# Performance work log

Hardware: AMD Instinct MI355X
Metric: run time of the kernel (lower is better)

The kernel has to match this reference:

```python
import jax, jax.numpy as jnp
import numpy as np

MAX_M = 16


def _twiddle(n, m):
    # exp(-2i*pi*n_a*m_a / (n*m)), shape (n, m), precomputed on host (static n, m)
    a = np.outer(np.arange(n), np.arange(m))
    return jnp.asarray(np.exp(-2j * np.pi * a / (n * m)).astype(np.complex64))


def _ref_dft_real(n, H):
    # reference DFT matrix as (H, n, n, 2) real view, matching ref_dft_matrix
    a = np.outer(np.arange(n), np.arange(n))
    M = np.exp(-2j * np.pi * a / n).astype(np.complex64)  # (n, n)
    M = np.broadcast_to(M, (H, n, n))
    return jnp.asarray(np.stack([M.real, M.imag], axis=-1).astype(np.float32))


def _cooley_tukey(k, n, m, mats):
    # k: (..., H, n*m) complex; mats[p]: (H, p, p) complex
    k = k.reshape(*k.shape[:-1], m, n)                      # (..., H, m, n)
    kf = jnp.einsum('hmo,...hon->...hmn', mats[m], k)       # m-length DFTs
    kf = jnp.einsum('nm,...mn->...nm', _twiddle(n, m), kf)  # twiddle + transpose -> (..., H, n, m)
    if n <= MAX_M:
        kf = jnp.einsum('hno,...hom->...hnm', mats[n], kf)  # n-length DFTs
    else:
        kf = jnp.moveaxis(kf, -1, -3)                        # '... h n m -> ... m h n'
        kf = _cooley_tukey(kf, n // MAX_M, MAX_M, mats)
        kf = jnp.moveaxis(kf, -3, -1)                        # '... m h n -> ... h n m'
    return kf.reshape(*kf.shape[:-2], n * m)


def block_fft(x, N, mats):
    # x: (..., H, L) complex, zero-pad to N, then recursive block FFT
    L = x.shape[-1]
    if L != N:
        x = jnp.pad(x, [(0, 0)] * (x.ndim - 1) + [(0, N - L)])
    return _cooley_tukey(x, N // MAX_M, MAX_M, mats)


def block_ifft(x, N, mats):
    return jnp.conj(block_fft(jnp.conj(x), N, mats)) / N


def setup_inputs() -> dict:
    key = jax.random.key(0)
    B, H, L = 16, 512, 1024
    ku, kk, kd = jax.random.split(key, 3)
    u = jax.random.normal(ku, (B, H, L), dtype=jnp.float32)
    k = jax.random.normal(kk, (H, L), dtype=jnp.float32) / L
    D = jax.random.normal(kd, (H,), dtype=jnp.float32)
    return {
        'u': u, 'k': k, 'D': D,
        'mat_2': _ref_dft_real(2, H),
        'mat_4': _ref_dft_real(4, H),
        'mat_8': _ref_dft_real(8, H),
        'mat_16': _ref_dft_real(16, H),
    }


def reference(u, k, D, mat_2, mat_4, mat_8, mat_16):
    cplx = lambda m: (m[..., 0] + 1j * m[..., 1]).astype(jnp.complex64)
    mats = {2: cplx(mat_2), 4: cplx(mat_4), 8: cplx(mat_8), 16: cplx(mat_16)}
    L = u.shape[-1]
    N = 2 * L  # causal FFT conv length
    k_f = block_fft(k.astype(jnp.complex64), N, mats)   # (H, N)
    u_f = block_fft(u.astype(jnp.complex64), N, mats)   # (B, H, N)
    y = block_ifft(u_f * k_f, N, mats)[..., :L].real    # (B, H, L)
    return (y + u * D[:, None]).astype(jnp.float32)
```

## Files before the change

### kernel.cpp

```cpp
#include <hip/hip_runtime.h>
#include <math.h>

#define NT     256
#define NB     16
#define NH     512
#define SEQ_L  1024
#define FFT_N  2048
#define RS     0.70710678118654752f

#define P(x) ((x) + ((x) >> 4))
#define BUF_SZ 2176

__device__ float2 g_kf[(size_t)NH * FFT_N];

__device__ __forceinline__ float2 cmul(float2 a, float2 b) {
    return make_float2(a.x * b.x - a.y * b.y, a.x * b.y + a.y * b.x);
}
__device__ __forceinline__ float2 cmulj(float2 a, float2 b) {
    return make_float2(a.x * b.x + a.y * b.y, a.y * b.x - a.x * b.y);
}
__device__ __forceinline__ float2 cadd(float2 a, float2 b) { return make_float2(a.x + b.x, a.y + b.y); }
__device__ __forceinline__ float2 csub(float2 a, float2 b) { return make_float2(a.x - b.x, a.y - b.y); }

template <int SIGN>
__device__ __forceinline__ void dft4(float2 x[4]) {
    float2 s0 = cadd(x[0], x[2]), s1 = csub(x[0], x[2]);
    float2 s2 = cadd(x[1], x[3]), s3 = csub(x[1], x[3]);
    x[0] = cadd(s0, s2);
    x[2] = csub(s0, s2);
    if (SIGN < 0) {
        x[1] = make_float2(s1.x + s3.y, s1.y - s3.x);
        x[3] = make_float2(s1.x - s3.y, s1.y + s3.x);
    } else {
        x[1] = make_float2(s1.x - s3.y, s1.y + s3.x);
        x[3] = make_float2(s1.x + s3.y, s1.y - s3.x);
    }
}

template <int SIGN>
__device__ __forceinline__ void dft8(float2 x[8]) {
    float2 e0 = cadd(x[0], x[4]), e1 = cadd(x[1], x[5]);
    float2 e2 = cadd(x[2], x[6]), e3 = cadd(x[3], x[7]);
    float2 o0 = csub(x[0], x[4]), o1 = csub(x[1], x[5]);
    float2 o2 = csub(x[2], x[6]), o3 = csub(x[3], x[7]);
    float2 t1, t2, t3;
    if (SIGN < 0) {
        t1 = make_float2(RS * (o1.x + o1.y), RS * (o1.y - o1.x));
        t2 = make_float2(o2.y, -o2.x);
        t3 = make_float2(-RS * (o3.x - o3.y), -RS * (o3.x + o3.y));
    } else {
        t1 = make_float2(RS * (o1.x - o1.y), RS * (o1.x + o1.y));
        t2 = make_float2(-o2.y, o2.x);
        t3 = make_float2(RS * (-o3.x - o3.y), RS * (o3.x - o3.y));
    }
    float2 s0 = cadd(e0, e2), s1 = csub(e0, e2), s2 = cadd(e1, e3), s3 = csub(e1, e3);
    x[0] = cadd(s0, s2);
    x[4] = csub(s0, s2);
    float2 u0 = cadd(o0, t2), u1 = csub(o0, t2), u2 = cadd(t1, t3), u3 = csub(t1, t3);
    x[1] = cadd(u0, u2);
    x[5] = csub(u0, u2);
    if (SIGN < 0) {
        x[2] = make_float2(s1.x + s3.y, s1.y - s3.x);
        x[6] = make_float2(s1.x - s3.y, s1.y + s3.x);
        x[3] = make_float2(u1.x + u3.y, u1.y - u3.x);
        x[7] = make_float2(u1.x - u3.y, u1.y + u3.x);
    } else {
        x[2] = make_float2(s1.x - s3.y, s1.y + s3.x);
        x[6] = make_float2(s1.x + s3.y, s1.y - s3.x);
        x[3] = make_float2(u1.x - u3.y, u1.y + u3.x);
        x[7] = make_float2(u1.x + u3.y, u1.y - u3.x);
    }
}

template <int SIGN>
__device__ __forceinline__ void stage8(float* re, float* im, const float2* tw,
                                       int t, int m, int twstep) {
    const int q = t & (m - 1);
    const int base = (t - q) * 8 + q;
    int idx[8];
    float2 x[8];
#pragma unroll
    for (int j = 0; j < 8; ++j) {
        idx[j] = P(base + j * m);
        x[j] = make_float2(re[idx[j]], im[idx[j]]);
    }
    const float2 w1 = tw[q * twstep];
    if (SIGN < 0) {
        dft8<-1>(x);
        float2 w = w1;
#pragma unroll
        for (int j = 1; j < 8; ++j) { x[j] = cmul(x[j], w); w = cmul(w, w1); }
    } else {
        float2 w = w1;
#pragma unroll
        for (int j = 1; j < 8; ++j) { x[j] = cmulj(x[j], w); w = cmul(w, w1); }
        dft8<+1>(x);
    }
#pragma unroll
    for (int j = 0; j < 8; ++j) { re[idx[j]] = x[j].x; im[idx[j]] = x[j].y; }
}

__device__ __forceinline__ void stage1_fwd(float* re, float* im, const float2* tw,
                                           int t, const float2 z[4]) {
    float2 e[4] = {z[0], z[1], z[2], z[3]};
    float2 o[4];
    o[0] = z[0];
    o[1] = make_float2(RS * (z[1].x + z[1].y), RS * (z[1].y - z[1].x));
    o[2] = make_float2(z[2].y, -z[2].x);
    o[3] = make_float2(-RS * (z[3].x - z[3].y), -RS * (z[3].x + z[3].y));
    dft4<-1>(e);
    dft4<-1>(o);
    float2 x[8] = {e[0], o[0], e[1], o[1], e[2], o[2], e[3], o[3]};
    const float2 w1 = tw[t];
    float2 w = w1;
#pragma unroll
    for (int j = 1; j < 8; ++j) { x[j] = cmul(x[j], w); w = cmul(w, w1); }
#pragma unroll
    for (int j = 0; j < 8; ++j) {
        const int id = P(t + j * 256);
        re[id] = x[j].x;
        im[id] = x[j].y;
    }
}

__global__ __launch_bounds__(NT, 8) void kfft_kernel(const float* __restrict__ kin) {
    __shared__ float re[BUF_SZ];
    __shared__ float im[BUF_SZ];
    __shared__ float2 tw[NT];
    const int t = threadIdx.x;
    const int h = blockIdx.x;
    {
        float sv, cv;
        sincosf(-6.283185307179586f * (float)t / (float)FFT_N, &sv, &cv);
        tw[t] = make_float2(cv, sv);
    }
    const float* krow = kin + (size_t)h * SEQ_L;
    float2 z[4];
#pragma unroll
    for (int l = 0; l < 4; ++l) z[l] = make_float2(krow[t + l * 256], 0.f);
    stage1_fwd(re, im, tw, t, z);
    __syncthreads();
    stage8<-1>(re, im, tw, t, 32, 8);
    __syncthreads();
    stage8<-1>(re, im, tw, t, 4, 64);
    __syncthreads();
    float2* out = g_kf + (size_t)h * FFT_N;
#pragma unroll
    for (int it = 0; it < 2; ++it) {
        const int b = t + it * NT;
        float2 x[4];
#pragma unroll
        for (int j = 0; j < 4; ++j) {
            const int id = P(4 * b + j);
            x[j] = make_float2(re[id], im[id]);
        }
        dft4<-1>(x);
#pragma unroll
        for (int j = 0; j < 4; ++j) out[4 * b + j] = x[j];
    }
}

__global__ __launch_bounds__(NT, 8) void conv_pair_kernel(const float* __restrict__ u,
                                                          const float* __restrict__ D,
                                                          float* __restrict__ out) {
    __shared__ float re[BUF_SZ];
    __shared__ float im[BUF_SZ];
    __shared__ float2 tw[NT];
    const int t = threadIdx.x;
    const int h = blockIdx.x & (NH - 1);
    const int bp = blockIdx.x >> 9;
    const size_t row0 = (size_t)(2 * bp) * NH + h;
    const size_t row1 = row0 + NH;
    {
        float sv, cv;
        sincosf(-6.283185307179586f * (float)t / (float)FFT_N, &sv, &cv);
        tw[t] = make_float2(cv, sv);
    }
    const float* u0 = u + row0 * SEQ_L;
    const float* u1 = u + row1 * SEQ_L;
    float ur0[4], ur1[4];
#pragma unroll
    for (int l = 0; l < 4; ++l) {
        ur0[l] = u0[t + l * 256];
        ur1[l] = u1[t + l * 256];
    }
    float2 z[4];
#pragma unroll
    for (int l = 0; l < 4; ++l) z[l] = make_float2(ur0[l], ur1[l]);
    stage1_fwd(re, im, tw, t, z);
    __syncthreads();
    stage8<-1>(re, im, tw, t, 32, 8);
    __syncthreads();
    stage8<-1>(re, im, tw, t, 4, 64);
    __syncthreads();
    const float2* kfr = g_kf + (size_t)h * FFT_N;
#pragma unroll
    for (int it = 0; it < 2; ++it) {
        const int b = t + it * NT;
        int id[4];
        float2 x[4];
#pragma unroll
        for (int j = 0; j < 4; ++j) {
            id[j] = P(4 * b + j);
            x[j] = make_float2(re[id[j]], im[id[j]]);
        }
        dft4<-1>(x);
#pragma unroll
        for (int j = 0; j < 4; ++j) x[j] = cmul(x[j], kfr[4 * b + j]);
        dft4<+1>(x);
#pragma unroll
        for (int j = 0; j < 4; ++j) { re[id[j]] = x[j].x; im[id[j]] = x[j].y; }
    }
    __syncthreads();
    stage8<+1>(re, im, tw, t, 4, 64);
    __syncthreads();
    stage8<+1>(re, im, tw, t, 32, 8);
    __syncthreads();
    float2 x[8];
#pragma unroll
    for (int j = 0; j < 8; ++j) {
        const int id = P(t + j * 256);
        x[j] = make_float2(re[id], im[id]);
    }
    {
        const float2 w1 = tw[t];
        float2 w = w1;
#pragma unroll
        for (int j = 1; j < 8; ++j) { x[j] = cmulj(x[j], w); w = cmul(w, w1); }
    }
    float2 e0 = cadd(x[0], x[4]), e1 = cadd(x[1], x[5]);
    float2 e2 = cadd(x[2], x[6]), e3 = cadd(x[3], x[7]);
    float2 o0 = csub(x[0], x[4]), o1 = csub(x[1], x[5]);
    float2 o2 = csub(x[2], x[6]), o3 = csub(x[3], x[7]);
    float2 t1 = make_float2(RS * (o1.x - o1.y), RS * (o1.x + o1.y));
    float2 t2 = make_float2(-o2.y, o2.x);
    float2 t3 = make_float2(RS * (-o3.x - o3.y), RS * (o3.x - o3.y));
    float2 s0 = cadd(e0, e2), s1 = csub(e0, e2), s2 = cadd(e1, e3), s3 = csub(e1, e3);
    float2 v0 = cadd(o0, t2), v1 = csub(o0, t2), v2 = cadd(t1, t3), v3 = csub(t1, t3);
    float2 y0 = cadd(s0, s2);
    float2 y1 = cadd(v0, v2);
    float2 y2 = make_float2(s1.x - s3.y, s1.y + s3.x);
    float2 y3 = make_float2(v1.x - v3.y, v1.y + v3.x);
    const float Dh = D[h];
    const float invN = 1.0f / (float)FFT_N;
    float* o0row = out + row0 * SEQ_L;
    float* o1row = out + row1 * SEQ_L;
    o0row[t]       = y0.x * invN + ur0[0] * Dh;
    o1row[t]       = y0.y * invN + ur1[0] * Dh;
    o0row[t + 256] = y1.x * invN + ur0[1] * Dh;
    o1row[t + 256] = y1.y * invN + ur1[1] * Dh;
    o0row[t + 512] = y2.x * invN + ur0[2] * Dh;
    o1row[t + 512] = y2.y * invN + ur1[2] * Dh;
    o0row[t + 768] = y3.x * invN + ur0[3] * Dh;
    o1row[t + 768] = y3.y * invN + ur1[3] * Dh;
}

extern "C" void kernel_launch(void* const* d_in, const int* in_sizes, int n_in,
                              void* d_out, int out_size, void* d_ws, size_t ws_size,
                              hipStream_t stream) {
    const float* u = (const float*)d_in[0];
    const float* k = (const float*)d_in[1];
    const float* D = (const float*)d_in[2];
    float* out = (float*)d_out;

    kfft_kernel<<<NH, NT, 0, stream>>>(k);
    conv_pair_kernel<<<NB * NH / 2, NT, 0, stream>>>(u, D, out);
}
```

Measured before the change: 118.6 us.

## Restructure FFT as radix-16x16x8 with 128 threads per block

Replaces the radix-8/8/8/4 staged FFT decomposition with a 16x16x8 factorization. The forward first stage exploits the zero padding, and the final inverse stage computes only the lower half of the outputs. Each thread now handles 16 points and block size drops from 256 to 128 threads, cutting the number of shared-memory passes and barriers. Kernel-spectrum reads and writes use float4. Costs include higher register pressure per thread and lower launch-bound occupancy.

```diff
diff --git a/kernel.cpp b/kernel.cpp
--- a/kernel.cpp
+++ b/kernel.cpp
@@ -1,17 +1,19 @@
 #include <hip/hip_runtime.h>
 #include <math.h>
 
-#define NT     256
+#define NT     128
 #define NB     16
 #define NH     512
 #define SEQ_L  1024
 #define FFT_N  2048
 #define RS     0.70710678118654752f
+#define C16    0.92387953251128675f
+#define S16    0.38268343236508977f
 
 #define P(x) ((x) + ((x) >> 4))
 #define BUF_SZ 2176
 
-__device__ float2 g_kf[(size_t)NH * FFT_N];
+__device__ __align__(16) float2 g_kf[(size_t)NH * FFT_N];
 
 __device__ __forceinline__ float2 cmul(float2 a, float2 b) {
     return make_float2(a.x * b.x - a.y * b.y, a.x * b.y + a.y * b.x);
@@ -73,186 +75,277 @@
 }
 
 template <int SIGN>
-__device__ __forceinline__ void stage8(float* re, float* im, const float2* tw,
-                                       int t, int m, int twstep) {
-    const int q = t & (m - 1);
-    const int base = (t - q) * 8 + q;
-    int idx[8];
-    float2 x[8];
-#pragma unroll
-    for (int j = 0; j < 8; ++j) {
-        idx[j] = P(base + j * m);
-        x[j] = make_float2(re[idx[j]], im[idx[j]]);
-    }
-    const float2 w1 = tw[q * twstep];
-    if (SIGN < 0) {
-        dft8<-1>(x);
-        float2 w = w1;
-#pragma unroll
-        for (int j = 1; j < 8; ++j) { x[j] = cmul(x[j], w); w = cmul(w, w1); }
-    } else {
-        float2 w = w1;
-#pragma unroll
-        for (int j = 1; j < 8; ++j) { x[j] = cmulj(x[j], w); w = cmul(w, w1); }
-        dft8<+1>(x);
-    }
-#pragma unroll
-    for (int j = 0; j < 8; ++j) { re[idx[j]] = x[j].x; im[idx[j]] = x[j].y; }
-}
-
-__device__ __forceinline__ void stage1_fwd(float* re, float* im, const float2* tw,
-                                           int t, const float2 z[4]) {
-    float2 e[4] = {z[0], z[1], z[2], z[3]};
-    float2 o[4];
-    o[0] = z[0];
-    o[1] = make_float2(RS * (z[1].x + z[1].y), RS * (z[1].y - z[1].x));
-    o[2] = make_float2(z[2].y, -z[2].x);
-    o[3] = make_float2(-RS * (z[3].x - z[3].y), -RS * (z[3].x + z[3].y));
-    dft4<-1>(e);
-    dft4<-1>(o);
-    float2 x[8] = {e[0], o[0], e[1], o[1], e[2], o[2], e[3], o[3]};
-    const float2 w1 = tw[t];
-    float2 w = w1;
-#pragma unroll
-    for (int j = 1; j < 8; ++j) { x[j] = cmul(x[j], w); w = cmul(w, w1); }
-#pragma unroll
-    for (int j = 0; j < 8; ++j) {
-        const int id = P(t + j * 256);
-        re[id] = x[j].x;
-        im[id] = x[j].y;
-    }
-}
-
-__global__ __launch_bounds__(NT, 8) void kfft_kernel(const float* __restrict__ kin) {
+__device__ __forceinline__ void dft16_twiddle(float2 v[4][4]) {
+    const float sg = (SIGN < 0) ? -1.f : 1.f;
+    const float2 W1 = make_float2(C16, sg * S16);
+    const float2 W2 = make_float2(RS, sg * RS);
+    const float2 W3 = make_float2(S16, sg * C16);
+    const float2 W6 = make_float2(-RS, sg * RS);
+    const float2 W9 = make_float2(-C16, -sg * S16);
+    v[1][1] = cmul(v[1][1], W1);
+    v[1][2] = cmul(v[1][2], W2);
+    v[1][3] = cmul(v[1][3], W3);
+    v[2][1] = cmul(v[2][1], W2);
+    v[2][2] = make_float2(-sg * v[2][2].y, sg * v[2][2].x);
+    v[2][3] = cmul(v[2][3], W6);
+    v[3][1] = cmul(v[3][1], W3);
+    v[3][2] = cmul(v[3][2], W6);
+    v[3][3] = cmul(v[3][3], W9);
+}
+
+template <int SIGN>
+__device__ __forceinline__ void dft16(float2 x[16]) {
+    float2 v[4][4];
+#pragma unroll
+    for (int n0 = 0; n0 < 4; ++n0) {
+        float2 a[4] = {x[n0], x[n0 + 4], x[n0 + 8], x[n0 + 12]};
+        dft4<SIGN>(a);
+        v[n0][0] = a[0]; v[n0][1] = a[1]; v[n0][2] = a[2]; v[n0][3] = a[3];
+    }
+    dft16_twiddle<SIGN>(v);
+#pragma unroll
+    for (int k0 = 0; k0 < 4; ++k0) {
+        float2 a[4] = {v[0][k0], v[1][k0], v[2][k0], v[3][k0]};
+        dft4<SIGN>(a);
+        x[k0] = a[0]; x[k0 + 4] = a[1]; x[k0 + 8] = a[2]; x[k0 + 12] = a[3];
+    }
+}
+
+__device__ __forceinline__ void dft16_zero8(const float2 z[8], float2 x[16]) {
+    float2 v[4][4];
+#pragma unroll
+    for (int n0 = 0; n0 < 4; ++n0) {
+        float2 a = z[n0], b = z[n0 + 4];
+        v[n0][0] = cadd(a, b);
+        v[n0][1] = make_float2(a.x + b.y, a.y - b.x);
+        v[n0][2] = csub(a, b);
+        v[n0][3] = make_float2(a.x - b.y, a.y + b.x);
+    }
+    dft16_twiddle<-1>(v);
+#pragma unroll
+    for (int k0 = 0; k0 < 4; ++k0) {
+        float2 a[4] = {v[0][k0], v[1][k0], v[2][k0], v[3][k0]};
+        dft4<-1>(a);
+        x[k0] = a[0]; x[k0 + 4] = a[1]; x[k0 + 8] = a[2]; x[k0 + 12] = a[3];
+    }
+}
+
+__device__ __forceinline__ void dft16_inv_low8(const float2 x[16], float2 y[8]) {
+    float2 v[4][4];
+#pragma unroll
+    for (int n0 = 0; n0 < 4; ++n0) {
+        float2 a[4] = {x[n0], x[n0 + 4], x[n0 + 8], x[n0 + 12]};
+        dft4<+1>(a);
+        v[n0][0] = a[0]; v[n0][1] = a[1]; v[n0][2] = a[2]; v[n0][3] = a[3];
+    }
+    dft16_twiddle<+1>(v);
+#pragma unroll
+    for (int k0 = 0; k0 < 4; ++k0) {
+        float2 x0 = v[0][k0], x1 = v[1][k0], x2 = v[2][k0], x3 = v[3][k0];
+        float2 s0 = cadd(x0, x2), s1 = csub(x0, x2);
+        float2 s2 = cadd(x1, x3), s3 = csub(x1, x3);
+        y[k0]     = cadd(s0, s2);
+        y[k0 + 4] = make_float2(s1.x - s3.y, s1.y + s3.x);
+    }
+}
+
+__global__ __launch_bounds__(NT, 4) void kfft_kernel(const float* __restrict__ kin) {
     __shared__ float re[BUF_SZ];
     __shared__ float im[BUF_SZ];
-    __shared__ float2 tw[NT];
+    __shared__ float2 twlds[NT];
     const int t = threadIdx.x;
     const int h = blockIdx.x;
+    float2 w1;
     {
         float sv, cv;
         sincosf(-6.283185307179586f * (float)t / (float)FFT_N, &sv, &cv);
-        tw[t] = make_float2(cv, sv);
+        w1 = make_float2(cv, sv);
+        twlds[t] = w1;
     }
     const float* krow = kin + (size_t)h * SEQ_L;
-    float2 z[4];
-#pragma unroll
-    for (int l = 0; l < 4; ++l) z[l] = make_float2(krow[t + l * 256], 0.f);
-    stage1_fwd(re, im, tw, t, z);
-    __syncthreads();
-    stage8<-1>(re, im, tw, t, 32, 8);
-    __syncthreads();
-    stage8<-1>(re, im, tw, t, 4, 64);
-    __syncthreads();
-    float2* out = g_kf + (size_t)h * FFT_N;
-#pragma unroll
-    for (int it = 0; it < 2; ++it) {
-        const int b = t + it * NT;
-        float2 x[4];
-#pragma unroll
-        for (int j = 0; j < 4; ++j) {
-            const int id = P(4 * b + j);
+    {
+        float2 z[8], x[16];
+#pragma unroll
+        for (int j = 0; j < 8; ++j) z[j] = make_float2(krow[t + 128 * j], 0.f);
+        dft16_zero8(z, x);
+        float2 w = w1;
+#pragma unroll
+        for (int c = 1; c < 16; ++c) { x[c] = cmul(x[c], w); w = cmul(w, w1); }
+#pragma unroll
+        for (int c = 0; c < 16; ++c) {
+            const int id = P(t + 128 * c);
+            re[id] = x[c].x; im[id] = x[c].y;
+        }
+    }
+    __syncthreads();
+    const int cblk = t >> 3, r = t & 7;
+    const int base = 128 * cblk + r;
+    {
+        float2 x[16];
+#pragma unroll
+        for (int j = 0; j < 16; ++j) {
+            const int id = P(base + 8 * j);
             x[j] = make_float2(re[id], im[id]);
         }
-        dft4<-1>(x);
-#pragma unroll
-        for (int j = 0; j < 4; ++j) out[4 * b + j] = x[j];
-    }
-}
-
-__global__ __launch_bounds__(NT, 8) void conv_pair_kernel(const float* __restrict__ u,
+        dft16<-1>(x);
+        const float2 ws = twlds[16 * r];
+        float2 w = ws;
+#pragma unroll
+        for (int c2 = 1; c2 < 16; ++c2) { x[c2] = cmul(x[c2], w); w = cmul(w, ws); }
+#pragma unroll
+        for (int c2 = 0; c2 < 16; ++c2) {
+            const int id = P(base + 8 * c2);
+            re[id] = x[c2].x; im[id] = x[c2].y;
+        }
+    }
+    __syncthreads();
+#pragma unroll
+    for (int gi = 0; gi < 2; ++gi) {
+        const int g = 2 * t + gi;
+        float2 x[8];
+#pragma unroll
+        for (int l = 0; l < 8; ++l) {
+            const int id = P(8 * g + l);
+            x[l] = make_float2(re[id], im[id]);
+        }
+        dft8<-1>(x);
+        float4* o4 = (float4*)(g_kf + (size_t)h * FFT_N + 8 * g);
+#pragma unroll
+        for (int l = 0; l < 4; ++l)
+            o4[l] = make_float4(x[2 * l].x, x[2 * l].y, x[2 * l + 1].x, x[2 * l + 1].y);
+    }
+}
+
+__global__ __launch_bounds__(NT, 4) void conv_pair_kernel(const float* __restrict__ u,
                                                           const float* __restrict__ D,
                                                           float* __restrict__ out) {
     __shared__ float re[BUF_SZ];
     __shared__ float im[BUF_SZ];
-    __shared__ float2 tw[NT];
+    __shared__ float2 twlds[NT];
     const int t = threadIdx.x;
     const int h = blockIdx.x & (NH - 1);
     const int bp = blockIdx.x >> 9;
     const size_t row0 = (size_t)(2 * bp) * NH + h;
     const size_t row1 = row0 + NH;
+    float2 w1;
     {
         float sv, cv;
         sincosf(-6.283185307179586f * (float)t / (float)FFT_N, &sv, &cv);
-        tw[t] = make_float2(cv, sv);
+        w1 = make_float2(cv, sv);
+        twlds[t] = w1;
     }
     const float* u0 = u + row0 * SEQ_L;
     const float* u1 = u + row1 * SEQ_L;
-    float ur0[4], ur1[4];
-#pragma unroll
-    for (int l = 0; l < 4; ++l) {
-        ur0[l] = u0[t + l * 256];
-        ur1[l] = u1[t + l * 256];
-    }
-    float2 z[4];
-#pragma unroll
-    for (int l = 0; l < 4; ++l) z[l] = make_float2(ur0[l], ur1[l]);
-    stage1_fwd(re, im, tw, t, z);
-    __syncthreads();
-    stage8<-1>(re, im, tw, t, 32, 8);
-    __syncthreads();
-    stage8<-1>(re, im, tw, t, 4, 64);
-    __syncthreads();
-    const float2* kfr = g_kf + (size_t)h * FFT_N;
-#pragma unroll
-    for (int it = 0; it < 2; ++it) {
-        const int b = t + it * NT;
-        int id[4];
-        float2 x[4];
-#pragma unroll
-        for (int j = 0; j < 4; ++j) {
-            id[j] = P(4 * b + j);
-            x[j] = make_float2(re[id[j]], im[id[j]]);
-        }
-        dft4<-1>(x);
-#pragma unroll
-        for (int j = 0; j < 4; ++j) x[j] = cmul(x[j], kfr[4 * b + j]);
-        dft4<+1>(x);
-#pragma unroll
-        for (int j = 0; j < 4; ++j) { re[id[j]] = x[j].x; im[id[j]] = x[j].y; }
-    }
-    __syncthreads();
-    stage8<+1>(re, im, tw, t, 4, 64);
-    __syncthreads();
-    stage8<+1>(re, im, tw, t, 32, 8);
-    __syncthreads();
-    float2 x[8];
+    float ur0[8], ur1[8];
 #pragma unroll
     for (int j = 0; j < 8; ++j) {
-        const int id = P(t + j * 256);
-        x[j] = make_float2(re[id], im[id]);
-    }
-    {
-        const float2 w1 = tw[t];
+        ur0[j] = u0[t + 128 * j];
+        ur1[j] = u1[t + 128 * j];
+    }
+    {
+        float2 z[8], x[16];
+#pragma unroll
+        for (int j = 0; j < 8; ++j) z[j] = make_float2(ur0[j], ur1[j]);
+        dft16_zero8(z, x);
         float2 w = w1;
 #pragma unroll
-        for (int j = 1; j < 8; ++j) { x[j] = cmulj(x[j], w); w = cmul(w, w1); }
-    }
-    float2 e0 = cadd(x[0], x[4]), e1 = cadd(x[1], x[5]);
-    float2 e2 = cadd(x[2], x[6]), e3 = cadd(x[3], x[7]);
-    float2 o0 = csub(x[0], x[4]), o1 = csub(x[1], x[5]);
-    float2 o2 = csub(x[2], x[6]), o3 = csub(x[3], x[7]);
-    float2 t1 = make_float2(RS * (o1.x - o1.y), RS * (o1.x + o1.y));
-    float2 t2 = make_float2(-o2.y, o2.x);
-    float2 t3 = make_float2(RS * (-o3.x - o3.y), RS * (o3.x - o3.y));
-    float2 s0 = cadd(e0, e2), s1 = csub(e0, e2), s2 = cadd(e1, e3), s3 = csub(e1, e3);
-    float2 v0 = cadd(o0, t2), v1 = csub(o0, t2), v2 = cadd(t1, t3), v3 = csub(t1, t3);
-    float2 y0 = cadd(s0, s2);
-    float2 y1 = cadd(v0, v2);
-    float2 y2 = make_float2(s1.x - s3.y, s1.y + s3.x);
-    float2 y3 = make_float2(v1.x - v3.y, v1.y + v3.x);
-    const float Dh = D[h];
-    const float invN = 1.0f / (float)FFT_N;
-    float* o0row = out + row0 * SEQ_L;
-    float* o1row = out + row1 * SEQ_L;
-    o0row[t]       = y0.x * invN + ur0[0] * Dh;
-    o1row[t]       = y0.y * invN + ur1[0] * Dh;
-    o0row[t + 256] = y1.x * invN + ur0[1] * Dh;
-    o1row[t + 256] = y1.y * invN + ur1[1] * Dh;
-    o0row[t + 512] = y2.x * invN + ur0[2] * Dh;
-    o1row[t + 512] = y2.y * invN + ur1[2] * Dh;
-    o0row[t + 768] = y3.x * invN + ur0[3] * Dh;
-    o1row[t + 768] = y3.y * invN + ur1[3] * Dh;
+        for (int c = 1; c < 16; ++c) { x[c] = cmul(x[c], w); w = cmul(w, w1); }
+#pragma unroll
+        for (int c = 0; c < 16; ++c) {
+            const int id = P(t + 128 * c);
+            re[id] = x[c].x; im[id] = x[c].y;
+        }
+    }
+    __syncthreads();
+    const int cblk = t >> 3, r = t & 7;
+    const int base = 128 * cblk + r;
+    const float2 ws = twlds[16 * r];
+    {
+        float2 x[16];
+#pragma unroll
+        for (int j = 0; j < 16; ++j) {
+            const int id = P(base + 8 * j);
+            x[j] = make_float2(re[id], im[id]);
+        }
+        dft16<-1>(x);
+        float2 w = ws;
+#pragma unroll
+        for (int c2 = 1; c2 < 16; ++c2) { x[c2] = cmul(x[c2], w); w = cmul(w, ws); }
+#pragma unroll
+        for (int c2 = 0; c2 < 16; ++c2) {
+            const int id = P(base + 8 * c2);
+            re[id] = x[c2].x; im[id] = x[c2].y;
+        }
+    }
+    __syncthreads();
+    {
+        const float2* kfr = g_kf + (size_t)h * FFT_N;
+#pragma unroll
+        for (int gi = 0; gi < 2; ++gi) {
+            const int g = 2 * t + gi;
+            float2 x[8];
+#pragma unroll
+            for (int l = 0; l < 8; ++l) {
+                const int id = P(8 * g + l);
+                x[l] = make_float2(re[id], im[id]);
+            }
+            dft8<-1>(x);
+            const float4* k4 = (const float4*)(kfr + 8 * g);
+#pragma unroll
+            for (int l = 0; l < 4; ++l) {
+                float4 kk = k4[l];
+                x[2 * l]     = cmul(x[2 * l],     make_float2(kk.x, kk.y));
+                x[2 * l + 1] = cmul(x[2 * l + 1], make_float2(kk.z, kk.w));
+            }
+            dft8<+1>(x);
+#pragma unroll
+            for (int l = 0; l < 8; ++l) {
+                const int id = P(8 * g + l);
+                re[id] = x[l].x; im[id] = x[l].y;
+            }
+        }
+    }
+    __syncthreads();
+    {
+        float2 x[16];
+#pragma unroll
+        for (int c2 = 0; c2 < 16; ++c2) {
+            const int id = P(base + 8 * c2);
+            x[c2] = make_float2(re[id], im[id]);
+        }
+        float2 w = ws;
+#pragma unroll
+        for (int c2 = 1; c2 < 16; ++c2) { x[c2] = cmulj(x[c2], w); w = cmul(w, ws); }
+        dft16<+1>(x);
+#pragma unroll
+        for (int j = 0; j < 16; ++j) {
+            const int id = P(base + 8 * j);
+            re[id] = x[j].x; im[id] = x[j].y;
+        }
+    }
+    __syncthreads();
+    {
+        float2 x[16];
+#pragma unroll
+        for (int c = 0; c < 16; ++c) {
+            const int id = P(t + 128 * c);
+            x[c] = make_float2(re[id], im[id]);
+        }
+        float2 w = w1;
+#pragma unroll
+        for (int c = 1; c < 16; ++c) { x[c] = cmulj(x[c], w); w = cmul(w, w1); }
+        float2 y[8];
+        dft16_inv_low8(x, y);
+        const float Dh = D[h];
+        const float invN = 1.0f / (float)FFT_N;
+        float* o0row = out + row0 * SEQ_L;
+        float* o1row = out + row1 * SEQ_L;
+#pragma unroll
+        for (int j = 0; j < 8; ++j) {
+            o0row[t + 128 * j] = y[j].x * invN + ur0[j] * Dh;
+            o1row[t + 128 * j] = y[j].y * invN + ur1[j] * Dh;
+        }
+    }
 }
 
 extern "C" void kernel_launch(void* const* d_in, const int* in_sizes, int n_in,
```

Result: slower. 137.8 us (+16.2%).
